# Optimization experiments

Measured on AMD Instinct MI355X. Metric: run time of the kernel, lower is better.

## Reference

```python
import jax, jax.numpy as jnp
import numpy as np

N = 100000       # num nodes
E = 1600000      # num edges (avg degree 16)
IN, HID, OUT, C = 128, 64, 64, 16


def setup_inputs() -> dict:
    key = jax.random.key(0)
    ks = jax.random.split(key, 10)
    x = jax.random.normal(ks[0], (N, IN), jnp.float32)
    edge_index = jax.random.randint(ks[1], (2, E), 0, N, dtype=jnp.int32)
    dict_node = jax.random.randint(ks[2], (N,), 0, N, dtype=jnp.int32)
    # learned parameters (Glorot-ish scaling)
    W1 = jax.random.normal(ks[3], (IN, HID), jnp.float32) / np.sqrt(IN)
    b1 = jnp.zeros((HID,), jnp.float32)
    W2 = jax.random.normal(ks[4], (HID, OUT), jnp.float32) / np.sqrt(HID)
    b2 = jnp.zeros((OUT,), jnp.float32)
    Wfc = jax.random.normal(ks[5], (OUT, C), jnp.float32) / np.sqrt(OUT)
    bfc = jnp.zeros((C,), jnp.float32)
    return {"x": x, "edge_index": edge_index, "dict_node": dict_node,
            "W1": W1, "b1": b1, "W2": W2, "b2": b2, "Wfc": Wfc, "bfc": bfc}


def _gcn_conv(h_in, W, b, src, dst, n):
    """GCNConv: D^-1/2 (A+I) D^-1/2 (X W) + b, self-loops handled analytically."""
    h = h_in @ W                                   # [N, F]
    deg = jax.ops.segment_sum(jnp.ones((src.shape[0],), h.dtype), dst,
                              num_segments=n) + 1.0  # +1 self-loop
    dinv = jax.lax.rsqrt(deg)                      # [N]
    norm = dinv[src] * dinv[dst]                   # [E]
    agg = jax.ops.segment_sum(h[src] * norm[:, None], dst, num_segments=n)
    agg = agg + h * (dinv * dinv)[:, None]         # self-loop contribution
    return agg + b


def reference(x, edge_index, dict_node, W1, b1, W2, b2, Wfc, bfc):
    n = x.shape[0]
    src, dst = edge_index[0], edge_index[1]
    h = jax.nn.relu(_gcn_conv(x, W1, b1, src, dst, n))
    # dropout p=0.5 is identity at inference
    h = jax.nn.relu(_gcn_conv(h, W2, b2, src, dst, n))
    # global_mean_pool over dict_node with size = num_nodes
    cnt = jax.ops.segment_sum(jnp.ones((n,), h.dtype), dict_node, num_segments=n)
    summ = jax.ops.segment_sum(h, dict_node, num_segments=n)
    pooled = summ / jnp.maximum(cnt, 1.0)[:, None]
    logits = pooled @ Wfc + bfc
    return jax.nn.log_softmax(logits, axis=1)
```

## Files before the change

kernel.cpp:

```cpp
#include <hip/hip_runtime.h>

#define THREADS 256
#define B1 256

typedef __attribute__((ext_vector_type(8))) short bf16x8;
typedef __attribute__((ext_vector_type(4))) float f32x4;
typedef __attribute__((ext_vector_type(2))) unsigned int u32x2;

__device__ inline ushort f2bf(float v) {
    union { float f; unsigned u; } a; a.f = v;
    unsigned r = a.u + 0x7fff + ((a.u >> 16) & 1);
    return (ushort)(r >> 16);
}
__device__ inline unsigned pack2(float a, float b) {
    return (unsigned)f2bf(a) | ((unsigned)f2bf(b) << 16);
}


__global__ void k_p1(const int* __restrict__ dst, int* __restrict__ pc,
                     int E, int NB, int chunk) {
    __shared__ int hist[512];
    int tid = threadIdx.x, blk = blockIdx.x;
    for (int i = tid; i < NB; i += THREADS) hist[i] = 0;
    __syncthreads();
    int e0 = blk * chunk;
    int e1 = e0 + chunk; if (e1 > E) e1 = E;
    for (int e = e0 + tid; e < e1; e += THREADS)
        atomicAdd(&hist[dst[e] >> 8], 1);
    __syncthreads();
    for (int i = tid; i < NB; i += THREADS) pc[i * B1 + blk] = hist[i];
}

__global__ void k_s1(int* __restrict__ pc, int* __restrict__ bsums, int total) {
    __shared__ int s[1024];
    int t = threadIdx.x;
    int idx = blockIdx.x * 1024 + t;
    int v = (idx < total) ? pc[idx] : 0;
    s[t] = v;
    __syncthreads();
    for (int o = 1; o < 1024; o <<= 1) {
        int x = (t >= (unsigned)o) ? s[t - o] : 0;
        __syncthreads();
        s[t] += x;
        __syncthreads();
    }
    if (idx < total) pc[idx] = s[t] - v;
    if (t == 1023) bsums[blockIdx.x] = s[1023];
}

__global__ void k_s2(int* __restrict__ bsums, int nb) {
    __shared__ int s[128];
    int t = threadIdx.x;
    int v = (t < nb) ? bsums[t] : 0;
    s[t] = v;
    __syncthreads();
    for (int o = 1; o < 128; o <<= 1) {
        int x = (t >= (unsigned)o) ? s[t - o] : 0;
        __syncthreads();
        s[t] += x;
        __syncthreads();
    }
    if (t < nb) bsums[t] = s[t] - v;
}

__global__ void k_p2(const int* __restrict__ src, const int* __restrict__ dst,
                     const int* __restrict__ pc, const int* __restrict__ bsx,
                     unsigned long long* __restrict__ part, int E, int NB, int chunk) {
    __shared__ int cur[512];
    int tid = threadIdx.x, blk = blockIdx.x;
    for (int i = tid; i < NB; i += THREADS) {
        int idx = i * B1 + blk;
        cur[i] = pc[idx] + bsx[idx >> 10];
    }
    __syncthreads();
    int e0 = blk * chunk;
    int e1 = e0 + chunk; if (e1 > E) e1 = E;
    for (int e = e0 + tid; e < e1; e += THREADS) {
        int d = dst[e], sv = src[e];
        int pos = atomicAdd(&cur[d >> 8], 1);
        part[pos] = ((unsigned long long)(unsigned)d << 32) | (unsigned)sv;
    }
}

__global__ void k_p3(const unsigned long long* __restrict__ part,
                     const int* __restrict__ pc, const int* __restrict__ bsx,
                     int* __restrict__ off, float* __restrict__ dinv,
                     int* __restrict__ csr, float* __restrict__ cnt,
                     int E, int NB, int n) {
    __shared__ int hist[256];
    __shared__ int so[256];
    int b = blockIdx.x, t = threadIdx.x;
    int i0 = b * B1, i1 = (b + 1) * B1;
    int base = pc[i0] + bsx[i0 >> 10];
    int end  = (b + 1 < NB) ? (pc[i1] + bsx[i1 >> 10]) : E;
    hist[t] = 0;
    __syncthreads();
    for (int e = base + t; e < end; e += THREADS)
        atomicAdd(&hist[(int)(part[e] >> 32) & 255], 1);
    __syncthreads();
    int h = hist[t];
    so[t] = h;
    __syncthreads();
    for (int o = 1; o < 256; o <<= 1) {
        int x = (t >= (unsigned)o) ? so[t - o] : 0;
        __syncthreads();
        so[t] += x;
        __syncthreads();
    }
    int ex = so[t] - h;
    int node = (b << 8) + t;
    if (node < n) {
        off[node]  = base + ex;
        dinv[node] = rsqrtf((float)h + 1.0f);
        cnt[node]  = 0.0f;
        if (node == n - 1) off[n] = E;
    }
    __syncthreads();
    so[t] = base + ex;
    __syncthreads();
    for (int e = base + t; e < end; e += THREADS) {
        unsigned long long p = part[e];
        int pos = atomicAdd(&so[(int)(p >> 32) & 255], 1);
        csr[pos] = (int)(p & 0xffffffffu);
    }
}

template<int KTILES, bool XF32>
__global__ __launch_bounds__(THREADS) void
k_mgemm(const float* __restrict__ Xf, const ushort* __restrict__ Xh,
        const float* __restrict__ W, const float* __restrict__ dinv,
        ushort* __restrict__ C, int n,
        const int* __restrict__ dict, float* __restrict__ cnt,
        float* __restrict__ pool16, int nGemm, int nCnt, int nZero) {
    int tid = threadIdx.x;
    if ((int)blockIdx.x >= nGemm) {
        int rb = (int)blockIdx.x - nGemm;
        if (rb < nCnt) {
            int stride = nCnt * THREADS;
            for (int i = rb * THREADS + tid; i < n; i += stride)
                atomicAdd(&cnt[dict[i]], 1.0f);
        } else {
            int zb = rb - nCnt;
            uint4* p4 = (uint4*)pool16;
            int tot = n * 4;
            int stride = nZero * THREADS;
            uint4 z = {0, 0, 0, 0};
            for (int i = zb * THREADS + tid; i < tot; i += stride) p4[i] = z;
        }
        return;
    }
    __shared__ ushort wfrag[KTILES * 2048];
    __shared__ float hrow[4][16 * 64];
    const int FIN = KTILES * 32;
    for (int i = tid; i < FIN * 64; i += THREADS) {
        int k = i >> 6, c = i & 63;
        int kk = k >> 5, G = (k >> 3) & 3, e = k & 7;
        int t = c >> 4, c16 = c & 15;
        wfrag[(((kk * 4 + t) * 64) + G * 16 + c16) * 8 + e] = f2bf(W[i]);
    }
    __syncthreads();
    int wslot = tid >> 6, lane = tid & 63;
    int G = lane >> 4, c16 = lane & 15;
    int n0 = blockIdx.x * 64 + wslot * 16;
    int xrow = n0 + c16; if (xrow >= n) xrow = n - 1;
    const bf16x8* wf = (const bf16x8*)wfrag;
    f32x4 acc0 = {0, 0, 0, 0}, acc1 = acc0, acc2 = acc0, acc3 = acc0;
    #pragma unroll
    for (int kk = 0; kk < KTILES; ++kk) {
        bf16x8 a;
        if (XF32) {
            const float* xp = Xf + (size_t)xrow * FIN + kk * 32 + G * 8;
            float4 xa = *(const float4*)xp;
            float4 xb = *(const float4*)(xp + 4);
            a[0] = (short)f2bf(xa.x); a[1] = (short)f2bf(xa.y);
            a[2] = (short)f2bf(xa.z); a[3] = (short)f2bf(xa.w);
            a[4] = (short)f2bf(xb.x); a[5] = (short)f2bf(xb.y);
            a[6] = (short)f2bf(xb.z); a[7] = (short)f2bf(xb.w);
        } else {
            a = *(const bf16x8*)(Xh + (size_t)xrow * FIN + kk * 32 + G * 8);
        }
        bf16x8 b0 = wf[(kk * 4 + 0) * 64 + lane];
        bf16x8 b1 = wf[(kk * 4 + 1) * 64 + lane];
        bf16x8 b2 = wf[(kk * 4 + 2) * 64 + lane];
        bf16x8 b3 = wf[(kk * 4 + 3) * 64 + lane];
        acc0 = __builtin_amdgcn_mfma_f32_16x16x32_bf16(a, b0, acc0, 0, 0, 0);
        acc1 = __builtin_amdgcn_mfma_f32_16x16x32_bf16(a, b1, acc1, 0, 0, 0);
        acc2 = __builtin_amdgcn_mfma_f32_16x16x32_bf16(a, b2, acc2, 0, 0, 0);
        acc3 = __builtin_amdgcn_mfma_f32_16x16x32_bf16(a, b3, acc3, 0, 0, 0);
    }
    int vm = n - n0; if (vm > 16) vm = 16;
    float* hr = &hrow[wslot][0];
    #pragma unroll
    for (int r = 0; r < 4; ++r) {
        int rr = G * 4 + r;
        if (rr < vm) {
            float dn = dinv[n0 + rr];
            hr[rr * 64 + c16]      = acc0[r] * dn;
            hr[rr * 64 + c16 + 16] = acc1[r] * dn;
            hr[rr * 64 + c16 + 32] = acc2[r] * dn;
            hr[rr * 64 + c16 + 48] = acc3[r] * dn;
        }
    }
    asm volatile("" ::: "memory");
    int prow = lane >> 2, pseg = lane & 3;
    if (prow < vm) {
        const float* hp = hr + prow * 64 + pseg * 16;
        float4 f0 = *(const float4*)(hp + 0);
        float4 f1 = *(const float4*)(hp + 4);
        float4 f2 = *(const float4*)(hp + 8);
        float4 f3 = *(const float4*)(hp + 12);
        uint4 o0, o1;
        o0.x = pack2(f0.x, f0.y); o0.y = pack2(f0.z, f0.w);
        o0.z = pack2(f1.x, f1.y); o0.w = pack2(f1.z, f1.w);
        o1.x = pack2(f2.x, f2.y); o1.y = pack2(f2.z, f2.w);
        o1.z = pack2(f3.x, f3.y); o1.w = pack2(f3.z, f3.w);
        ushort* op = C + ((size_t)(n0 + prow) << 6) + pseg * 16;
        *(uint4*)(op)     = o0;
        *(uint4*)(op + 8) = o1;
    }
}

__device__ inline void tr_mfma4(unsigned la, const bf16x8& a,
                                f32x4& o0, f32x4& o1, f32x4& o2, f32x4& o3) {
    u32x2 r0, r1, r2, r3, r4, r5, r6, r7;
    asm volatile(
        "s_waitcnt lgkmcnt(0)\n\t"
        "ds_read_b64_tr_b16 %0, %8 offset:0\n\t"
        "ds_read_b64_tr_b16 %1, %8 offset:512\n\t"
        "ds_read_b64_tr_b16 %2, %8 offset:1024\n\t"
        "ds_read_b64_tr_b16 %3, %8 offset:1536\n\t"
        "ds_read_b64_tr_b16 %4, %8 offset:2048\n\t"
        "ds_read_b64_tr_b16 %5, %8 offset:2560\n\t"
        "ds_read_b64_tr_b16 %6, %8 offset:3072\n\t"
        "ds_read_b64_tr_b16 %7, %8 offset:3584\n\t"
        "s_waitcnt lgkmcnt(0)"
        : "=&v"(r0), "=&v"(r1), "=&v"(r2), "=&v"(r3),
          "=&v"(r4), "=&v"(r5), "=&v"(r6), "=&v"(r7)
        : "v"(la) : "memory");
    __builtin_amdgcn_sched_barrier(0);
    union { u32x2 d[2]; bf16x8 v; } b0, b1, b2, b3;
    b0.d[0] = r0; b0.d[1] = r1; b1.d[0] = r2; b1.d[1] = r3;
    b2.d[0] = r4; b2.d[1] = r5; b3.d[0] = r6; b3.d[1] = r7;
    o0 = __builtin_amdgcn_mfma_f32_16x16x32_bf16(a, b0.v, o0, 0, 0, 0);
    o1 = __builtin_amdgcn_mfma_f32_16x16x32_bf16(a, b1.v, o1, 0, 0, 0);
    o2 = __builtin_amdgcn_mfma_f32_16x16x32_bf16(a, b2.v, o2, 0, 0, 0);
    o3 = __builtin_amdgcn_mfma_f32_16x16x32_bf16(a, b3.v, o3, 0, 0, 0);
}

template<int LAYER>
__global__ __launch_bounds__(THREADS) void
k_agg(const ushort* __restrict__ H, const int* __restrict__ csr,
      const int* __restrict__ off, const float* __restrict__ dinv,
      const float* __restrict__ bias, ushort* __restrict__ outB,
      const float* __restrict__ wsrc, const int* __restrict__ dict,
      float* __restrict__ pool16, int n) {
    __shared__ ushort cbuf[4][2048];
    __shared__ ushort extra[LAYER == 1 ? 4096 : 2080];
    int tid = threadIdx.x;
    if (LAYER == 1) {
        for (int i = tid; i < 64 * 64; i += THREADS) {
            int k = i >> 6, c = i & 63;
            int kk = k >> 5, Gs = (k >> 3) & 3, e = k & 7;
            int t = c >> 4, cs = c & 15;
            extra[(((kk * 4 + t) * 64) + Gs * 16 + cs) * 8 + e] = f2bf(wsrc[i]);
        }
        __syncthreads();
    } else {
        float* wt = (float*)extra;
        for (int i = tid; i < 64 * 16; i += THREADS) {
            int cc = i >> 4, r = i & 15;
            wt[r * 65 + cc] = wsrc[i];
        }
        __syncthreads();
    }
    int wslot = tid >> 6, lane = tid & 63;
    int gw = blockIdx.x * 4 + wslot;
    int n0 = gw << 4;
    if (n0 >= n) return;
    int G = lane >> 4, c16 = lane & 15;
    int g8 = lane >> 3, q = lane & 7;
    ushort* wbuf = &cbuf[wslot][0];
    unsigned lbase = (unsigned)(size_t)wbuf;
    int vm = n - n0; if (vm > 16) vm = 16;
    int sA = 0, eA = 0;
    if (c16 < vm) { sA = off[n0 + c16]; eA = off[n0 + c16 + 1]; }
    int base0   = __shfl(sA, 0);
    int baseEnd = __shfl(eA, vm - 1);
    unsigned rng = (unsigned)(eA - sA);
    int sb0 = (q >> 1) * 512 + (g8 >> 2) * 256 + (g8 & 3) * 16 + (q & 1) * 8;
    unsigned la = lbase + (unsigned)lane * 8;
    f32x4 acc0 = {0, 0, 0, 0}, acc1 = acc0, acc2 = acc0, acc3 = acc0;

    uint4 c0[4], c1[4], c2[4];
    #pragma unroll
    for (int it = 0; it < 4; ++it) {
        uint4 v = {0, 0, 0, 0};
        int k = base0 + it * 8 + g8;
        if (k < baseEnd) {
            int e = csr[k];
            v = *(const uint4*)(H + ((size_t)e << 6) + q * 8);
        }
        c0[it] = v;
    }
    #pragma unroll
    for (int it = 0; it < 4; ++it) {
        uint4 v = {0, 0, 0, 0};
        int k = base0 + 32 + it * 8 + g8;
        if (k < baseEnd) {
            int e = csr[k];
            v = *(const uint4*)(H + ((size_t)e << 6) + q * 8);
        }
        c1[it] = v;
    }
    for (int base = base0; base < baseEnd; base += 32) {
        #pragma unroll
        for (int it = 0; it < 4; ++it) {
            uint4 v = {0, 0, 0, 0};
            int k = base + 64 + it * 8 + g8;
            if (k < baseEnd) {
                int e = csr[k];
                v = *(const uint4*)(H + ((size_t)e << 6) + q * 8);
            }
            c2[it] = v;
        }
        #pragma unroll
        for (int it = 0; it < 4; ++it)
            *(uint4*)(wbuf + sb0 + it * 64) = c0[it];
        int kb = base - sA;
        bf16x8 a;
        #pragma unroll
        for (int e2 = 0; e2 < 8; ++e2)
            a[e2] = ((unsigned)(G * 8 + e2 + kb) < rng) ? (short)0x3F80 : (short)0;
        tr_mfma4(la, a, acc0, acc1, acc2, acc3);
        #pragma unroll
        for (int it = 0; it < 4; ++it) { c0[it] = c1[it]; c1[it] = c2[it]; }
    }
    {
        #pragma unroll
        for (int it = 0; it < 4; ++it) {
            uint4 v = {0, 0, 0, 0};
            int k = it * 8 + g8;
            if (it < 2 && k < vm)
                v = *(const uint4*)(H + ((size_t)(n0 + k) << 6) + q * 8);
            *(uint4*)(wbuf + sb0 + it * 64) = v;
        }
        bf16x8 a;
        #pragma unroll
        for (int e2 = 0; e2 < 8; ++e2)
            a[e2] = ((G * 8 + e2) == c16) ? (short)0x3F80 : (short)0;
        tr_mfma4(la, a, acc0, acc1, acc2, acc3);
    }
    float* hrow = (float*)wbuf;
    float bv0 = bias[c16], bv1 = bias[c16 + 16],
          bv2 = bias[c16 + 32], bv3 = bias[c16 + 48];
    #pragma unroll
    for (int r = 0; r < 4; ++r) {
        int rr = G * 4 + r;
        if (rr < vm) {
            float dn = dinv[n0 + rr];
            float v0 = fmaxf(acc0[r] * dn + bv0, 0.f);
            float v1 = fmaxf(acc1[r] * dn + bv1, 0.f);
            float v2 = fmaxf(acc2[r] * dn + bv2, 0.f);
            float v3 = fmaxf(acc3[r] * dn + bv3, 0.f);
            hrow[rr * 64 + c16]      = v0;
            hrow[rr * 64 + c16 + 16] = v1;
            hrow[rr * 64 + c16 + 32] = v2;
            hrow[rr * 64 + c16 + 48] = v3;
        }
    }
    asm volatile("" ::: "memory");
    if (LAYER == 1) {
        const float* ap = hrow + c16 * 64 + G * 8;
        float4 xa = *(const float4*)(ap);
        float4 xb = *(const float4*)(ap + 4);
        float4 ya = *(const float4*)(ap + 32);
        float4 yb = *(const float4*)(ap + 36);
        bf16x8 a0, a1;
        a0[0] = (short)f2bf(xa.x); a0[1] = (short)f2bf(xa.y);
        a0[2] = (short)f2bf(xa.z); a0[3] = (short)f2bf(xa.w);
        a0[4] = (short)f2bf(xb.x); a0[5] = (short)f2bf(xb.y);
        a0[6] = (short)f2bf(xb.z); a0[7] = (short)f2bf(xb.w);
        a1[0] = (short)f2bf(ya.x); a1[1] = (short)f2bf(ya.y);
        a1[2] = (short)f2bf(ya.z); a1[3] = (short)f2bf(ya.w);
        a1[4] = (short)f2bf(yb.x); a1[5] = (short)f2bf(yb.y);
        a1[6] = (short)f2bf(yb.z); a1[7] = (short)f2bf(yb.w);
        const bf16x8* wf2 = (const bf16x8*)extra;
        f32x4 h0 = {0, 0, 0, 0}, h1v = h0, h2v = h0, h3v = h0;
        h0  = __builtin_amdgcn_mfma_f32_16x16x32_bf16(a0, wf2[0 * 64 + lane], h0, 0, 0, 0);
        h1v = __builtin_amdgcn_mfma_f32_16x16x32_bf16(a0, wf2[1 * 64 + lane], h1v, 0, 0, 0);
        h2v = __builtin_amdgcn_mfma_f32_16x16x32_bf16(a0, wf2[2 * 64 + lane], h2v, 0, 0, 0);
        h3v = __builtin_amdgcn_mfma_f32_16x16x32_bf16(a0, wf2[3 * 64 + lane], h3v, 0, 0, 0);
        h0  = __builtin_amdgcn_mfma_f32_16x16x32_bf16(a1, wf2[4 * 64 + lane], h0, 0, 0, 0);
        h1v = __builtin_amdgcn_mfma_f32_16x16x32_bf16(a1, wf2[5 * 64 + lane], h1v, 0, 0, 0);
        h2v = __builtin_amdgcn_mfma_f32_16x16x32_bf16(a1, wf2[6 * 64 + lane], h2v, 0, 0, 0);
        h3v = __builtin_amdgcn_mfma_f32_16x16x32_bf16(a1, wf2[7 * 64 + lane], h3v, 0, 0, 0);
        asm volatile("" ::: "memory");
        #pragma unroll
        for (int r = 0; r < 4; ++r) {
            int rr = G * 4 + r;
            if (rr < vm) {
                float dn = dinv[n0 + rr];
                hrow[rr * 64 + c16]      = h0[r] * dn;
                hrow[rr * 64 + c16 + 16] = h1v[r] * dn;
                hrow[rr * 64 + c16 + 32] = h2v[r] * dn;
                hrow[rr * 64 + c16 + 48] = h3v[r] * dn;
            }
        }
        asm volatile("" ::: "memory");
        int prow = lane >> 2, pseg = lane & 3;
        if (prow < vm) {
            const float* hp = hrow + prow * 64 + pseg * 16;
            float4 f0 = *(const float4*)(hp + 0);
            float4 f1 = *(const float4*)(hp + 4);
            float4 f2 = *(const float4*)(hp + 8);
            float4 f3 = *(const float4*)(hp + 12);
            uint4 o0, o1;
            o0.x = pack2(f0.x, f0.y); o0.y = pack2(f0.z, f0.w);
            o0.z = pack2(f1.x, f1.y); o0.w = pack2(f1.z, f1.w);
            o1.x = pack2(f2.x, f2.y); o1.y = pack2(f2.z, f2.w);
            o1.z = pack2(f3.x, f3.y); o1.w = pack2(f3.z, f3.w);
            ushort* op = outB + ((size_t)(n0 + prow) << 6) + pseg * 16;
            *(uint4*)(op)     = o0;
            *(uint4*)(op + 8) = o1;
        }
    } else {
        const float* wt = (const float*)extra;
        int r16 = c16;
        for (int m = 0; m < vm; ++m) {
            const float* hm = hrow + m * 64 + G * 16;
            const float* wr = wt + r16 * 65 + G * 16;
            float p = 0.f;
            #pragma unroll
            for (int i = 0; i < 16; ++i) p = fmaf(hm[i], wr[i], p);
            p += __shfl_xor(p, 16);
            p += __shfl_xor(p, 32);
            if (G == 0)
                atomicAdd(&pool16[(size_t)dict[n0 + m] * 16 + r16], p);
        }
    }
}

__global__ void k_final16(const float* __restrict__ pool16, const float* __restrict__ cnt,
                          const float* __restrict__ bfc, float* __restrict__ out, int n) {
    int tid = threadIdx.x;
    int nl = tid >> 4, lane = tid & 15;
    int node = blockIdx.x * 16 + nl;
    if (node >= n) return;
    float inv = 1.0f / fmaxf(cnt[node], 1.0f);
    float acc = pool16[(size_t)node * 16 + lane] * inv + bfc[lane];
    float m = acc;
    for (int o = 8; o; o >>= 1) m = fmaxf(m, __shfl_xor(m, o, 16));
    float ex = __expf(acc - m);
    float s = ex;
    for (int o = 8; o; o >>= 1) s += __shfl_xor(s, o, 16);
    out[(size_t)node * 16 + lane] = acc - m - __logf(s);
}

extern "C" void kernel_launch(void* const* d_in, const int* in_sizes, int n_in,
                              void* d_out, int out_size, void* d_ws, size_t ws_size,
                              hipStream_t stream) {
    const float* x    = (const float*)d_in[0];
    const int*   ei   = (const int*)d_in[1];
    const int*   dict = (const int*)d_in[2];
    const float* W1   = (const float*)d_in[3];
    const float* b1   = (const float*)d_in[4];
    const float* W2   = (const float*)d_in[5];
    const float* b2   = (const float*)d_in[6];
    const float* Wfc  = (const float*)d_in[7];
    const float* bfc  = (const float*)d_in[8];

    const int N  = in_sizes[2];
    const int E  = in_sizes[1] / 2;
    const int IN = in_sizes[0] / N;
    const int* src = ei;
    const int* dst = ei + E;

    ushort* bufA = (ushort*)d_ws;
    ushort* bufB = bufA + (size_t)N * 64;
    unsigned long long* part = (unsigned long long*)bufB;
    float* dinv    = (float*)(bufB + (size_t)N * 64);
    float* cnt     = dinv + N;
    int*   off     = (int*)(cnt + N);
    int*   pcounts = off + (N + 1);
    const int NB     = (N + 255) >> 8;
    const int pcsize = NB * B1;
    int*   bsums   = pcounts + pcsize;
    int*   csr     = bsums + 128;
    float* pool16  = (float*)(csr + E);

    const int gTile = (N + 63) / 64;
    const int gRows = (N + 15) / 16;
    const int nCnt  = 256;
    const int nZero = 256;
    const int chunk = (E + B1 - 1) / B1;
    const int nS1   = (pcsize + 1023) >> 10;
    const int gAgg  = ((N + 15) / 16 + 3) / 4;

    k_p1<<<B1, THREADS, 0, stream>>>(dst, pcounts, E, NB, chunk);
    k_s1<<<nS1, 1024, 0, stream>>>(pcounts, bsums, pcsize);
    k_s2<<<1, 128, 0, stream>>>(bsums, nS1);
    k_p2<<<B1, THREADS, 0, stream>>>(src, dst, pcounts, bsums, part, E, NB, chunk);
    k_p3<<<NB, THREADS, 0, stream>>>(part, pcounts, bsums, off, dinv, csr, cnt,
                                     E, NB, N);

    k_mgemm<4, true><<<gTile + nCnt + nZero, THREADS, 0, stream>>>(
        x, nullptr, W1, dinv, bufA, N, dict, cnt, pool16, gTile, nCnt, nZero);

    k_agg<1><<<gAgg, THREADS, 0, stream>>>(bufA, csr, off, dinv, b1, bufB,
                                           W2, nullptr, nullptr, N);

    k_agg<2><<<gAgg, THREADS, 0, stream>>>(bufB, csr, off, dinv, b2, nullptr,
                                           Wfc, dict, pool16, N);

    k_final16<<<gRows, THREADS, 0, stream>>>(pool16, cnt, bfc, (float*)d_out, N);
}
```

Baseline: 271.2 us.

## Halve nodes per wave in aggregation and preconvert W2 outside agg kernels

Each wave in the aggregation kernels now handles 8 destination nodes instead of 16, doubling the grid. This gives more parallelism and shorter per-wave edge loops. W2 is converted to the bf16 MFMA layout once, inside the small scan kernel, and read from global memory, which removes the per-block LDS setup and barrier. Wfc is loaded into registers rather than a transposed LDS table. The trade-off is that the MFMA tiles are now half empty (rows 8-15 are zeroed), so matrix work per node effectively doubles.

```diff
diff --git a/kernel.cpp b/kernel.cpp
--- a/kernel.cpp
+++ b/kernel.cpp
@@ -48,7 +48,8 @@
     if (t == 1023) bsums[blockIdx.x] = s[1023];
 }
 
-__global__ void k_s2(int* __restrict__ bsums, int nb) {
+__global__ void k_s2(int* __restrict__ bsums, int nb,
+                     const float* __restrict__ W2, ushort* __restrict__ w2f) {
     __shared__ int s[128];
     int t = threadIdx.x;
     int v = (t < nb) ? bsums[t] : 0;
@@ -61,6 +62,12 @@
         __syncthreads();
     }
     if (t < nb) bsums[t] = s[t] - v;
+    for (int i = t; i < 64 * 64; i += 128) {
+        int k = i >> 6, c = i & 63;
+        int kk = k >> 5, Gs = (k >> 3) & 3, e = k & 7;
+        int tt = c >> 4, cs = c & 15;
+        w2f[(((kk * 4 + tt) * 64) + Gs * 16 + cs) * 8 + e] = f2bf(W2[i]);
+    }
 }
 
 __global__ void k_p2(const int* __restrict__ src, const int* __restrict__ dst,
@@ -252,36 +259,19 @@
 k_agg(const ushort* __restrict__ H, const int* __restrict__ csr,
       const int* __restrict__ off, const float* __restrict__ dinv,
       const float* __restrict__ bias, ushort* __restrict__ outB,
-      const float* __restrict__ wsrc, const int* __restrict__ dict,
-      float* __restrict__ pool16, int n) {
+      const ushort* __restrict__ w2f, const float* __restrict__ Wfc,
+      const int* __restrict__ dict, float* __restrict__ pool16, int n) {
     __shared__ ushort cbuf[4][2048];
-    __shared__ ushort extra[LAYER == 1 ? 4096 : 2080];
     int tid = threadIdx.x;
-    if (LAYER == 1) {
-        for (int i = tid; i < 64 * 64; i += THREADS) {
-            int k = i >> 6, c = i & 63;
-            int kk = k >> 5, Gs = (k >> 3) & 3, e = k & 7;
-            int t = c >> 4, cs = c & 15;
-            extra[(((kk * 4 + t) * 64) + Gs * 16 + cs) * 8 + e] = f2bf(wsrc[i]);
-        }
-        __syncthreads();
-    } else {
-        float* wt = (float*)extra;
-        for (int i = tid; i < 64 * 16; i += THREADS) {
-            int cc = i >> 4, r = i & 15;
-            wt[r * 65 + cc] = wsrc[i];
-        }
-        __syncthreads();
-    }
     int wslot = tid >> 6, lane = tid & 63;
     int gw = blockIdx.x * 4 + wslot;
-    int n0 = gw << 4;
+    int n0 = gw << 3;
     if (n0 >= n) return;
     int G = lane >> 4, c16 = lane & 15;
     int g8 = lane >> 3, q = lane & 7;
     ushort* wbuf = &cbuf[wslot][0];
     unsigned lbase = (unsigned)(size_t)wbuf;
-    int vm = n - n0; if (vm > 16) vm = 16;
+    int vm = n - n0; if (vm > 8) vm = 8;
     int sA = 0, eA = 0;
     if (c16 < vm) { sA = off[n0 + c16]; eA = off[n0 + c16 + 1]; }
     int base0   = __shfl(sA, 0);
@@ -340,7 +330,7 @@
         for (int it = 0; it < 4; ++it) {
             uint4 v = {0, 0, 0, 0};
             int k = it * 8 + g8;
-            if (it < 2 && k < vm)
+            if (k < vm)
                 v = *(const uint4*)(H + ((size_t)(n0 + k) << 6) + q * 8);
             *(uint4*)(wbuf + sb0 + it * 64) = v;
         }
@@ -368,6 +358,10 @@
             hrow[rr * 64 + c16 + 48] = v3;
         }
     }
+    if (LAYER == 1) {
+        #pragma unroll
+        for (int r = 8; r < 16; ++r) hrow[r * 64 + lane] = 0.f;
+    }
     asm volatile("" ::: "memory");
     if (LAYER == 1) {
         const float* ap = hrow + c16 * 64 + G * 8;
@@ -384,7 +378,7 @@
         a1[2] = (short)f2bf(ya.z); a1[3] = (short)f2bf(ya.w);
         a1[4] = (short)f2bf(yb.x); a1[5] = (short)f2bf(yb.y);
         a1[6] = (short)f2bf(yb.z); a1[7] = (short)f2bf(yb.w);
-        const bf16x8* wf2 = (const bf16x8*)extra;
+        const bf16x8* wf2 = (const bf16x8*)w2f;
         f32x4 h0 = {0, 0, 0, 0}, h1v = h0, h2v = h0, h3v = h0;
         h0  = __builtin_amdgcn_mfma_f32_16x16x32_bf16(a0, wf2[0 * 64 + lane], h0, 0, 0, 0);
         h1v = __builtin_amdgcn_mfma_f32_16x16x32_bf16(a0, wf2[1 * 64 + lane], h1v, 0, 0, 0);
@@ -424,18 +418,19 @@
             *(uint4*)(op + 8) = o1;
         }
     } else {
-        const float* wt = (const float*)extra;
-        int r16 = c16;
+        float wr[16];
+        #pragma unroll
+        for (int i = 0; i < 16; ++i)
+            wr[i] = Wfc[(G * 16 + i) * 16 + c16];
         for (int m = 0; m < vm; ++m) {
             const float* hm = hrow + m * 64 + G * 16;
-            const float* wr = wt + r16 * 65 + G * 16;
             float p = 0.f;
             #pragma unroll
             for (int i = 0; i < 16; ++i) p = fmaf(hm[i], wr[i], p);
             p += __shfl_xor(p, 16);
             p += __shfl_xor(p, 32);
             if (G == 0)
-                atomicAdd(&pool16[(size_t)dict[n0 + m] * 16 + r16], p);
+                atomicAdd(&pool16[(size_t)dict[n0 + m] * 16 + c16], p);
         }
     }
 }
@@ -487,6 +482,7 @@
     int*   bsums   = pcounts + pcsize;
     int*   csr     = bsums + 128;
     float* pool16  = (float*)(csr + E);
+    ushort* w2f    = (ushort*)(pool16 + (size_t)N * 16);
 
     const int gTile = (N + 63) / 64;
     const int gRows = (N + 15) / 16;
@@ -494,11 +490,11 @@
     const int nZero = 256;
     const int chunk = (E + B1 - 1) / B1;
     const int nS1   = (pcsize + 1023) >> 10;
-    const int gAgg  = ((N + 15) / 16 + 3) / 4;
+    const int gAgg  = ((N + 7) / 8 + 3) / 4;
 
     k_p1<<<B1, THREADS, 0, stream>>>(dst, pcounts, E, NB, chunk);
     k_s1<<<nS1, 1024, 0, stream>>>(pcounts, bsums, pcsize);
-    k_s2<<<1, 128, 0, stream>>>(bsums, nS1);
+    k_s2<<<1, 128, 0, stream>>>(bsums, nS1, W2, w2f);
     k_p2<<<B1, THREADS, 0, stream>>>(src, dst, pcounts, bsums, part, E, NB, chunk);
     k_p3<<<NB, THREADS, 0, stream>>>(part, pcounts, bsums, off, dinv, csr, cnt,
                                      E, NB, N);
@@ -507,10 +503,10 @@
         x, nullptr, W1, dinv, bufA, N, dict, cnt, pool16, gTile, nCnt, nZero);
 
     k_agg<1><<<gAgg, THREADS, 0, stream>>>(bufA, csr, off, dinv, b1, bufB,
-                                           W2, nullptr, nullptr, N);
+                                           w2f, nullptr, nullptr, nullptr, N);
 
     k_agg<2><<<gAgg, THREADS, 0, stream>>>(bufB, csr, off, dinv, b2, nullptr,
-                                           Wfc, dict, pool16, N);
+                                           nullptr, Wfc, dict, pool16, N);
 
     k_final16<<<gRows, THREADS, 0, stream>>>(pool16, cnt, bfc, (float*)d_out, N);
 }
```

Result: no change. 274.4 us (+1.2%).
